# Kernel tuning notes

Hardware: AMD Instinct MI355X
Metric: run time of the kernel (lower is better)

The kernel has to match this reference:

```python
import jax, jax.numpy as jnp
import numpy as np

B, D = 16384, 1024
N_CROSS = 3
EPS = 1e-3  # keras BatchNormalization default epsilon


def _bn(x, gamma, beta, mean, var):
    # inference-mode batch norm over feature axis
    return gamma * (x - mean) * jax.lax.rsqrt(var + EPS) + beta


def setup_inputs() -> dict:
    key = jax.random.key(0)
    ks = jax.random.split(key, 16)
    s = lambda fan_in: 1.0 / np.sqrt(fan_in)
    inp = {
        "x": jax.random.normal(ks[0], (B, D), jnp.float32),
        "cross_w": jax.random.normal(ks[1], (N_CROSS, D), jnp.float32) * s(D),
        "cross_b": jax.random.normal(ks[2], (N_CROSS, D), jnp.float32) * 0.01,
        "w1": jax.random.normal(ks[3], (D, 64), jnp.float32) * s(D),
        "b1": jnp.zeros((64,), jnp.float32),
        "gamma1": jnp.ones((64,), jnp.float32),
        "beta1": jnp.zeros((64,), jnp.float32),
        "mean1": jax.random.normal(ks[4], (64,), jnp.float32) * 0.1,
        "var1": jax.random.uniform(ks[5], (64,), jnp.float32, 0.5, 1.5),
        "w2": jax.random.normal(ks[6], (64, 48), jnp.float32) * s(64),
        "b2": jnp.zeros((48,), jnp.float32),
        "gamma2": jnp.ones((48,), jnp.float32),
        "beta2": jnp.zeros((48,), jnp.float32),
        "mean2": jax.random.normal(ks[7], (48,), jnp.float32) * 0.1,
        "var2": jax.random.uniform(ks[8], (48,), jnp.float32, 0.5, 1.5),
        "w3": jax.random.normal(ks[9], (48, 24), jnp.float32) * s(48),
        "b3": jnp.zeros((24,), jnp.float32),
        "gamma3": jnp.ones((24,), jnp.float32),
        "beta3": jnp.zeros((24,), jnp.float32),
        "mean3": jax.random.normal(ks[10], (24,), jnp.float32) * 0.1,
        "var3": jax.random.uniform(ks[11], (24,), jnp.float32, 0.5, 1.5),
        "w_out": jax.random.normal(ks[12], (D + 24, 1), jnp.float32) * s(D + 24),
        "b_out": jnp.zeros((1,), jnp.float32),
    }
    return inp


def reference(x, cross_w, cross_b, w1, b1, gamma1, beta1, mean1, var1,
              w2, b2, gamma2, beta2, mean2, var2,
              w3, b3, gamma3, beta3, mean3, var3, w_out, b_out):
    # ---- cross network: xl = x0 * (xl . w) + b + xl ----
    # Algebraically identical to matmul(x0[:,:,None], xl[:,None,:]) @ w,
    # computed in O(B*D) instead of materializing [B, D, D].
    x0 = x
    xl = x
    for i in range(N_CROSS):
        scal = jnp.einsum('bd,d->b', xl, cross_w[i])  # [B]
        xl = x0 * scal[:, None] + cross_b[i] + xl
    # ---- deep tower (inference: dropout is identity, BN uses moving stats) ----
    h = _bn(jax.nn.relu(x @ w1 + b1), gamma1, beta1, mean1, var1)
    h = _bn(jnp.tanh(h @ w2 + b2), gamma2, beta2, mean2, var2)
    h = _bn(jnp.tanh(h @ w3 + b3), gamma3, beta3, mean3, var3)
    out = jnp.concatenate([xl, h], axis=1)           # [B, D+24]
    return jax.nn.sigmoid(out @ w_out + b_out)       # [B, 1]
```

## Files before the change

kernel.cpp:

```cpp
#include <hip/hip_runtime.h>
#include <hip/hip_bf16.h>
#include <math.h>

typedef __attribute__((ext_vector_type(8))) short bf16x8;
typedef __attribute__((ext_vector_type(4))) float f32x4;

constexpr int BD = 1024;
constexpr float EPS = 1e-3f;
constexpr int WB_MAIN = 32 * 5 * 64 * 8 * 2;
constexpr int WB2_OFF = WB_MAIN;
constexpr int WB3_OFF = WB2_OFF + 6144;
constexpr int CST_OFF = WB3_OFF + 4096;

__device__ __forceinline__ float wave_allsum(float v) {
#pragma unroll
    for (int m = 1; m < 64; m <<= 1) v += __shfl_xor(v, m, 64);
    return v;
}
__device__ __forceinline__ unsigned short f2bf(float f) {
    __hip_bfloat16 h = __float2bfloat16(f);
    unsigned short u; __builtin_memcpy(&u, &h, 2);
    return u;
}
__device__ __forceinline__ float bf2f(unsigned short u) {
    return __uint_as_float(((unsigned)u) << 16);
}
__device__ __forceinline__ float tanh_fast(float x) {
    const float xc = fminf(fmaxf(x, -15.f), 15.f);
    const float e = __expf(2.f * xc);
    return (e - 1.f) * __builtin_amdgcn_rcpf(e + 1.f);
}
__device__ __forceinline__ float sigmoid_fast(float z) {
    return __builtin_amdgcn_rcpf(1.f + __expf(-z));
}

__global__ void dcn_prep(const float* __restrict__ w1,
                         const float* __restrict__ cross_w,
                         const float* __restrict__ cross_b,
                         const float* __restrict__ w_out,
                         const float* __restrict__ w2,
                         const float* __restrict__ w3,
                         unsigned short* __restrict__ ws) {
    const int bx = blockIdx.x;
    if (bx == 40) {
        if (threadIdx.x < 64) {
            const int l = threadIdx.x;
            float q2 = 0.f, q3 = 0.f, Cc = 0.f;
            for (int j = 0; j < 16; ++j) {
                const int k = l * 16 + j;
                const float c0 = cross_b[k], c1 = cross_b[BD + k], c2 = cross_b[2 * BD + k];
                q2 += c0 * cross_w[BD + k];
                q3 += (c0 + c1) * cross_w[2 * BD + k];
                Cc += (c0 + c1 + c2) * w_out[k];
            }
            q2 = wave_allsum(q2); q3 = wave_allsum(q3); Cc = wave_allsum(Cc);
            float* consts = (float*)((char*)ws + CST_OFF);
            if (l == 0) { consts[0] = q2; consts[1] = q3; consts[2] = Cc; }
        }
        return;
    }
    if (bx < 40) {
        const int idx = bx * 256 + threadIdx.x;
        const int g = idx / 320;
        const int rem = idx - g * 320;
        const int t = rem >> 6;
        const int l = rem & 63;
        const int c = l & 15;
        const int k0 = g * 32 + (l >> 4) * 8;
        unsigned short o[8] __attribute__((aligned(16)));
#pragma unroll
        for (int j = 0; j < 8; ++j) {
            const int k = k0 + j;
            unsigned short r;
            if (t < 4) {
                r = f2bf(w1[k * 64 + t * 16 + c]);
            } else if (c < 8) {
                const int vsel = c & 3;
                const float v = (vsel < 3) ? cross_w[vsel * BD + k] : w_out[k];
                const unsigned short h = f2bf(v);
                r = (c < 4) ? h : f2bf(v - bf2f(h));
            } else {
                r = 0;
            }
            o[j] = r;
        }
        *(uint4*)(ws + (size_t)idx * 8) = *(const uint4*)o;
        return;
    }
    const int slot = (bx - 41) * 256 + threadIdx.x;
    if (slot < 384) {
        const int f = slot >> 6, l = slot & 63;
        const int K = f / 3, T = f % 3;
        const int kb = K * 32 + (l >> 4) * 8;
        const int col = T * 16 + (l & 15);
        unsigned short o[8] __attribute__((aligned(16)));
#pragma unroll
        for (int j = 0; j < 8; ++j) o[j] = f2bf(w2[(kb + j) * 48 + col]);
        unsigned short* wb2 = (unsigned short*)((char*)ws + WB2_OFF);
        *(uint4*)(wb2 + (size_t)slot * 8) = *(const uint4*)o;
    } else if (slot < 640) {
        const int s2 = slot - 384;
        const int f = s2 >> 6, l = s2 & 63;
        const int K = f >> 1, T = f & 1;
        const int kb = K * 32 + (l >> 4) * 8;
        const int col = T * 16 + (l & 15);
        unsigned short o[8] __attribute__((aligned(16)));
#pragma unroll
        for (int j = 0; j < 8; ++j) {
            const int k = kb + j;
            o[j] = (k < 48 && col < 24) ? f2bf(w3[k * 24 + col]) : (unsigned short)0;
        }
        unsigned short* wb3 = (unsigned short*)((char*)ws + WB3_OFF);
        *(uint4*)(wb3 + (size_t)s2 * 8) = *(const uint4*)o;
    }
}

__global__ __launch_bounds__(64, 1) void dcn_main(
    const float* __restrict__ x,
    const unsigned short* __restrict__ wbm,
    const unsigned short* __restrict__ w2f,
    const unsigned short* __restrict__ w3f,
    const float* __restrict__ consts,
    const float* __restrict__ b1, const float* __restrict__ g1,
    const float* __restrict__ be1, const float* __restrict__ m1, const float* __restrict__ v1,
    const float* __restrict__ b2, const float* __restrict__ g2,
    const float* __restrict__ be2, const float* __restrict__ m2, const float* __restrict__ v2,
    const float* __restrict__ b3, const float* __restrict__ g3,
    const float* __restrict__ be3, const float* __restrict__ m3, const float* __restrict__ v3,
    const float* __restrict__ w_out, const float* __restrict__ b_out,
    float* __restrict__ out)
{
    __shared__ char sb[8960] __attribute__((aligned(16)));
    constexpr int H1 = 0, H2 = 4352, LC = 8704;

    const int l = threadIdx.x;
    const int ar = l & 15;
    const int ag = l >> 4;
    const int gr0 = blockIdx.x * 16;

    const float* xbase = x + (size_t)(gr0 + ar) * BD + ag * 8;
    const bf16x8* bb = (const bf16x8*)wbm + l;

    const float q2c = consts[0], q3c = consts[1], Ccc = consts[2];
    const float bo = b_out[0];
    const float wo0 = w_out[1024 + ar];
    const float wo1 = (ar < 8) ? w_out[1040 + ar] : 0.f;
    float b1p[4], g1p[4], be1p[4], m1p[4], iv1p[4];
#pragma unroll
    for (int t = 0; t < 4; ++t) {
        const int c = t * 16 + ar;
        b1p[t] = b1[c]; g1p[t] = g1[c]; be1p[t] = be1[c]; m1p[t] = m1[c];
        iv1p[t] = rsqrtf(v1[c] + EPS);
    }

    float4 A0[6], A1[6];
#pragma unroll
    for (int s = 0; s < 6; ++s) {
        A0[s] = *(const float4*)(xbase + s * 32);
        A1[s] = *(const float4*)(xbase + s * 32 + 4);
    }
    bf16x8 Bf[4][5];
#pragma unroll
    for (int s = 0; s < 4; ++s)
#pragma unroll
        for (int t = 0; t < 5; ++t) Bf[s][t] = bb[(s * 5 + t) * 64];

    f32x4 acc0 = {0.f,0.f,0.f,0.f}, acc1 = acc0, acc2 = acc0, acc3 = acc0, acc4 = acc0;

#pragma unroll
    for (int s = 0; s < 32; ++s) {
        const float4 va0 = A0[s % 6];
        const float4 va1 = A1[s % 6];
        if (s + 6 < 32) {
            A0[s % 6] = *(const float4*)(xbase + (s + 6) * 32);
            A1[s % 6] = *(const float4*)(xbase + (s + 6) * 32 + 4);
        }
        const bf16x8 B0 = Bf[s & 3][0], B1 = Bf[s & 3][1], B2 = Bf[s & 3][2],
                     B3 = Bf[s & 3][3], B4 = Bf[s & 3][4];
        if (s + 4 < 32) {
#pragma unroll
            for (int t = 0; t < 5; ++t) Bf[s & 3][t] = bb[((s + 4) * 5 + t) * 64];
        }
        bf16x8 xh, xl;
#define CVT(F, I) { const unsigned short h_ = f2bf(F); xh[I] = (short)h_; \
                    xl[I] = (short)f2bf((F) - bf2f(h_)); }
        CVT(va0.x, 0) CVT(va0.y, 1) CVT(va0.z, 2) CVT(va0.w, 3)
        CVT(va1.x, 4) CVT(va1.y, 5) CVT(va1.z, 6) CVT(va1.w, 7)
#undef CVT
        acc0 = __builtin_amdgcn_mfma_f32_16x16x32_bf16(xh, B0, acc0, 0, 0, 0);
        acc1 = __builtin_amdgcn_mfma_f32_16x16x32_bf16(xh, B1, acc1, 0, 0, 0);
        acc2 = __builtin_amdgcn_mfma_f32_16x16x32_bf16(xh, B2, acc2, 0, 0, 0);
        acc3 = __builtin_amdgcn_mfma_f32_16x16x32_bf16(xh, B3, acc3, 0, 0, 0);
        acc4 = __builtin_amdgcn_mfma_f32_16x16x32_bf16(xh, B4, acc4, 0, 0, 0);
        acc4 = __builtin_amdgcn_mfma_f32_16x16x32_bf16(xl, B4, acc4, 0, 0, 0);
    }

    const bf16x8* w2b = (const bf16x8*)w2f + l;
    bf16x8 W2[6];
#pragma unroll
    for (int f = 0; f < 6; ++f) W2[f] = w2b[f * 64];
    const bf16x8* w3b = (const bf16x8*)w3f + l;
    bf16x8 W3[4];
#pragma unroll
    for (int f = 0; f < 4; ++f) W3[f] = w3b[f * 64];
    float b2p[3], g2p[3], be2p[3], m2p[3], iv2p[3];
#pragma unroll
    for (int t = 0; t < 3; ++t) {
        const int c = t * 16 + ar;
        b2p[t] = b2[c]; g2p[t] = g2[c]; be2p[t] = be2[c]; m2p[t] = m2[c];
        iv2p[t] = rsqrtf(v2[c] + EPS);
    }
    float b3p[2], g3p[2], be3p[2], m3p[2], iv3p[2];
#pragma unroll
    for (int t = 0; t < 2; ++t) {
        const int c = t == 0 ? ar : (16 + ar < 24 ? 16 + ar : 23);
        b3p[t] = b3[c]; g3p[t] = g3[c]; be3p[t] = be3[c]; m3p[t] = m3[c];
        iv3p[t] = rsqrtf(v3[c] + EPS);
    }

    {
        f32x4 p4 = acc4;
#pragma unroll
        for (int q = 0; q < 4; ++q) p4[q] += __shfl_xor(acc4[q], 4, 64);
        if (ar < 4) {
#pragma unroll
            for (int q = 0; q < 4; ++q)
                *(float*)&sb[LC + ((ag * 4 + q) * 4 + ar) * 4] = p4[q];
        }
    }

    {
        const f32x4 av[4] = {acc0, acc1, acc2, acc3};
#pragma unroll
        for (int t = 0; t < 4; ++t) {
            const int c = t * 16 + ar;
#pragma unroll
            for (int q = 0; q < 4; ++q) {
                const float y = fmaxf(av[t][q] + b1p[t], 0.f);
                const float h = fmaf(g1p[t] * (y - m1p[t]), iv1p[t], be1p[t]);
                *(float*)&sb[H1 + (ag * 4 + q) * 272 + c * 4] = h;
            }
        }
    }
    {
        const f32x4 z4 = {0.f, 0.f, 0.f, 0.f};
        *(f32x4*)&sb[H2 + ar * 272 + 192 + ag * 16] = z4;
    }

    bf16x8 a2[2];
#pragma unroll
    for (int K = 0; K < 2; ++K) {
        const float4 f0 = *(const float4*)&sb[H1 + ar * 272 + (K * 32 + ag * 8) * 4];
        const float4 f1 = *(const float4*)&sb[H1 + ar * 272 + (K * 32 + ag * 8) * 4 + 16];
        const float v[8] = {f0.x, f0.y, f0.z, f0.w, f1.x, f1.y, f1.z, f1.w};
#pragma unroll
        for (int i = 0; i < 8; ++i) a2[K][i] = (short)f2bf(v[i]);
    }
    f32x4 c2t[3] = {{0.f,0.f,0.f,0.f},{0.f,0.f,0.f,0.f},{0.f,0.f,0.f,0.f}};
#pragma unroll
    for (int K = 0; K < 2; ++K) {
        c2t[0] = __builtin_amdgcn_mfma_f32_16x16x32_bf16(a2[K], W2[K * 3 + 0], c2t[0], 0, 0, 0);
        c2t[1] = __builtin_amdgcn_mfma_f32_16x16x32_bf16(a2[K], W2[K * 3 + 1], c2t[1], 0, 0, 0);
        c2t[2] = __builtin_amdgcn_mfma_f32_16x16x32_bf16(a2[K], W2[K * 3 + 2], c2t[2], 0, 0, 0);
    }
#pragma unroll
    for (int t = 0; t < 3; ++t) {
        const int c = t * 16 + ar;
#pragma unroll
        for (int q = 0; q < 4; ++q) {
            const float th = tanh_fast(c2t[t][q] + b2p[t]);
            const float h = fmaf(g2p[t] * (th - m2p[t]), iv2p[t], be2p[t]);
            *(float*)&sb[H2 + (ag * 4 + q) * 272 + c * 4] = h;
        }
    }

    bf16x8 a3[2];
#pragma unroll
    for (int K = 0; K < 2; ++K) {
        const float4 f0 = *(const float4*)&sb[H2 + ar * 272 + (K * 32 + ag * 8) * 4];
        const float4 f1 = *(const float4*)&sb[H2 + ar * 272 + (K * 32 + ag * 8) * 4 + 16];
        const float v[8] = {f0.x, f0.y, f0.z, f0.w, f1.x, f1.y, f1.z, f1.w};
#pragma unroll
        for (int i = 0; i < 8; ++i) a3[K][i] = (short)f2bf(v[i]);
    }
    f32x4 c3t[2] = {{0.f,0.f,0.f,0.f},{0.f,0.f,0.f,0.f}};
#pragma unroll
    for (int K = 0; K < 2; ++K) {
        c3t[0] = __builtin_amdgcn_mfma_f32_16x16x32_bf16(a3[K], W3[K * 2 + 0], c3t[0], 0, 0, 0);
        c3t[1] = __builtin_amdgcn_mfma_f32_16x16x32_bf16(a3[K], W3[K * 2 + 1], c3t[1], 0, 0, 0);
    }
    float contrib[4];
#pragma unroll
    for (int q = 0; q < 4; ++q) {
        const float t0 = tanh_fast(c3t[0][q] + b3p[0]);
        const float h0 = fmaf(g3p[0] * (t0 - m3p[0]), iv3p[0], be3p[0]);
        const float t1 = tanh_fast(c3t[1][q] + b3p[1]);
        const float h1v = fmaf(g3p[1] * (t1 - m3p[1]), iv3p[1], be3p[1]);
        contrib[q] = h0 * wo0 + h1v * wo1;
    }
#pragma unroll
    for (int m = 1; m < 16; m <<= 1) {
#pragma unroll
        for (int q = 0; q < 4; ++q) contrib[q] += __shfl_xor(contrib[q], m, 64);
    }

#pragma unroll
    for (int q = 0; q < 4; ++q) {
        const f32x4 pr = *(const f32x4*)&sb[LC + (ag * 4 + q) * 16];
        const float p1 = pr[0], p2 = pr[1], p3 = pr[2], d0 = pr[3];
        const float s1 = p1;
        const float s2 = fmaf(1.f + s1, p2, q2c);
        const float s3 = fmaf(1.f + s1 + s2, p3, q3c);
        const float alpha = 1.f + s1 + s2 + s3;
        const float z = fmaf(alpha, d0, Ccc) + contrib[q] + bo;
        const float o = sigmoid_fast(z);
        if (ar == q) out[gr0 + ag * 4 + q] = o;
    }
}

extern "C" void kernel_launch(void* const* d_in, const int* in_sizes, int n_in,
                              void* d_out, int out_size, void* d_ws, size_t ws_size,
                              hipStream_t stream) {
    const float* x       = (const float*)d_in[0];
    const float* cross_w = (const float*)d_in[1];
    const float* cross_b = (const float*)d_in[2];
    const float* w1      = (const float*)d_in[3];
    const float* b1      = (const float*)d_in[4];
    const float* g1      = (const float*)d_in[5];
    const float* be1     = (const float*)d_in[6];
    const float* m1      = (const float*)d_in[7];
    const float* v1      = (const float*)d_in[8];
    const float* w2      = (const float*)d_in[9];
    const float* b2      = (const float*)d_in[10];
    const float* g2      = (const float*)d_in[11];
    const float* be2     = (const float*)d_in[12];
    const float* m2      = (const float*)d_in[13];
    const float* v2      = (const float*)d_in[14];
    const float* w3      = (const float*)d_in[15];
    const float* b3      = (const float*)d_in[16];
    const float* g3      = (const float*)d_in[17];
    const float* be3     = (const float*)d_in[18];
    const float* m3      = (const float*)d_in[19];
    const float* v3      = (const float*)d_in[20];
    const float* w_out   = (const float*)d_in[21];
    const float* b_out   = (const float*)d_in[22];
    float* out = (float*)d_out;

    unsigned short* ws = (unsigned short*)d_ws;
    const unsigned short* w2f = (const unsigned short*)((char*)d_ws + WB2_OFF);
    const unsigned short* w3f = (const unsigned short*)((char*)d_ws + WB3_OFF);
    const float* consts = (const float*)((char*)d_ws + CST_OFF);

    dcn_prep<<<44, 256, 0, stream>>>(w1, cross_w, cross_b, w_out, w2, w3, ws);
    dcn_main<<<1024, 64, 0, stream>>>(x, ws, w2f, w3f, consts,
                                      b1, g1, be1, m1, v1,
                                      b2, g2, be2, m2, v2,
                                      b3, g3, be3, m3, v3,
                                      w_out, b_out, out);
}
```

Measured before the change: 25.98 us.

## Split K dimension across two waves per block with LDS reduction

Each block now runs two wavefronts. Each wave processes half of the 1024-wide K dimension for the same 16 rows, and the second wave's MFMA accumulators are reduced into the first wave through shared memory before the tail stages run. This doubles the number of waves streaming x from memory and halves the serial MFMA chain per wave, aiming to hide load latency better. In exchange it adds an LDS round trip, a barrier, and a second wave that sits idle during the tail work.

```diff
diff --git a/kernel.cpp b/kernel.cpp
--- a/kernel.cpp
+++ b/kernel.cpp
@@ -115,7 +115,7 @@
     }
 }
 
-__global__ __launch_bounds__(64, 1) void dcn_main(
+__global__ __launch_bounds__(128, 2) void dcn_main(
     const float* __restrict__ x,
     const unsigned short* __restrict__ wbm,
     const unsigned short* __restrict__ w2f,
@@ -130,32 +130,22 @@
     const float* __restrict__ w_out, const float* __restrict__ b_out,
     float* __restrict__ out)
 {
-    __shared__ char sb[8960] __attribute__((aligned(16)));
-    constexpr int H1 = 0, H2 = 4352, LC = 8704;
-
-    const int l = threadIdx.x;
+    __shared__ char sb[14336] __attribute__((aligned(16)));
+    constexpr int RED = 0, H1 = 5120, H2 = 9472, LC = 13824;
+
+    const int tid = threadIdx.x;
+    const int l = tid & 63;
+    const int w = tid >> 6;
     const int ar = l & 15;
     const int ag = l >> 4;
     const int gr0 = blockIdx.x * 16;
 
-    const float* xbase = x + (size_t)(gr0 + ar) * BD + ag * 8;
-    const bf16x8* bb = (const bf16x8*)wbm + l;
-
-    const float q2c = consts[0], q3c = consts[1], Ccc = consts[2];
-    const float bo = b_out[0];
-    const float wo0 = w_out[1024 + ar];
-    const float wo1 = (ar < 8) ? w_out[1040 + ar] : 0.f;
-    float b1p[4], g1p[4], be1p[4], m1p[4], iv1p[4];
-#pragma unroll
-    for (int t = 0; t < 4; ++t) {
-        const int c = t * 16 + ar;
-        b1p[t] = b1[c]; g1p[t] = g1[c]; be1p[t] = be1[c]; m1p[t] = m1[c];
-        iv1p[t] = rsqrtf(v1[c] + EPS);
-    }
-
-    float4 A0[6], A1[6];
-#pragma unroll
-    for (int s = 0; s < 6; ++s) {
+    const float* xbase = x + (size_t)(gr0 + ar) * BD + w * 512 + ag * 8;
+    const bf16x8* bb = (const bf16x8*)wbm + (size_t)(w * 16 * 5) * 64 + l;
+
+    float4 A0[8], A1[8];
+#pragma unroll
+    for (int s = 0; s < 8; ++s) {
         A0[s] = *(const float4*)(xbase + s * 32);
         A1[s] = *(const float4*)(xbase + s * 32 + 4);
     }
@@ -168,16 +158,16 @@
     f32x4 acc0 = {0.f,0.f,0.f,0.f}, acc1 = acc0, acc2 = acc0, acc3 = acc0, acc4 = acc0;
 
 #pragma unroll
-    for (int s = 0; s < 32; ++s) {
-        const float4 va0 = A0[s % 6];
-        const float4 va1 = A1[s % 6];
-        if (s + 6 < 32) {
-            A0[s % 6] = *(const float4*)(xbase + (s + 6) * 32);
-            A1[s % 6] = *(const float4*)(xbase + (s + 6) * 32 + 4);
+    for (int s = 0; s < 16; ++s) {
+        const float4 va0 = A0[s & 7];
+        const float4 va1 = A1[s & 7];
+        if (s < 8) {
+            A0[s & 7] = *(const float4*)(xbase + (s + 8) * 32);
+            A1[s & 7] = *(const float4*)(xbase + (s + 8) * 32 + 4);
         }
         const bf16x8 B0 = Bf[s & 3][0], B1 = Bf[s & 3][1], B2 = Bf[s & 3][2],
                      B3 = Bf[s & 3][3], B4 = Bf[s & 3][4];
-        if (s + 4 < 32) {
+        if (s + 4 < 16) {
 #pragma unroll
             for (int t = 0; t < 5; ++t) Bf[s & 3][t] = bb[((s + 4) * 5 + t) * 64];
         }
@@ -195,6 +185,22 @@
         acc4 = __builtin_amdgcn_mfma_f32_16x16x32_bf16(xl, B4, acc4, 0, 0, 0);
     }
 
+    if (w == 1) {
+        *(f32x4*)&sb[RED + 0 * 1024 + l * 16] = acc0;
+        *(f32x4*)&sb[RED + 1 * 1024 + l * 16] = acc1;
+        *(f32x4*)&sb[RED + 2 * 1024 + l * 16] = acc2;
+        *(f32x4*)&sb[RED + 3 * 1024 + l * 16] = acc3;
+        *(f32x4*)&sb[RED + 4 * 1024 + l * 16] = acc4;
+    }
+    __syncthreads();
+    if (w == 1) return;
+
+    acc0 += *(const f32x4*)&sb[RED + 0 * 1024 + l * 16];
+    acc1 += *(const f32x4*)&sb[RED + 1 * 1024 + l * 16];
+    acc2 += *(const f32x4*)&sb[RED + 2 * 1024 + l * 16];
+    acc3 += *(const f32x4*)&sb[RED + 3 * 1024 + l * 16];
+    acc4 += *(const f32x4*)&sb[RED + 4 * 1024 + l * 16];
+
     const bf16x8* w2b = (const bf16x8*)w2f + l;
     bf16x8 W2[6];
 #pragma unroll
@@ -203,6 +209,18 @@
     bf16x8 W3[4];
 #pragma unroll
     for (int f = 0; f < 4; ++f) W3[f] = w3b[f * 64];
+
+    const float q2c = consts[0], q3c = consts[1], Ccc = consts[2];
+    const float bo = b_out[0];
+    const float wo0 = w_out[1024 + ar];
+    const float wo1 = (ar < 8) ? w_out[1040 + ar] : 0.f;
+    float b1p[4], g1p[4], be1p[4], m1p[4], iv1p[4];
+#pragma unroll
+    for (int t = 0; t < 4; ++t) {
+        const int c = t * 16 + ar;
+        b1p[t] = b1[c]; g1p[t] = g1[c]; be1p[t] = be1[c]; m1p[t] = m1[c];
+        iv1p[t] = rsqrtf(v1[c] + EPS);
+    }
     float b2p[3], g2p[3], be2p[3], m2p[3], iv2p[3];
 #pragma unroll
     for (int t = 0; t < 3; ++t) {
@@ -352,9 +370,9 @@
     const float* consts = (const float*)((char*)d_ws + CST_OFF);
 
     dcn_prep<<<44, 256, 0, stream>>>(w1, cross_w, cross_b, w_out, w2, w3, ws);
-    dcn_main<<<1024, 64, 0, stream>>>(x, ws, w2f, w3f, consts,
-                                      b1, g1, be1, m1, v1,
-                                      b2, g2, be2, m2, v2,
-                                      b3, g3, be3, m3, v3,
-                                      w_out, b_out, out);
-}
+    dcn_main<<<1024, 128, 0, stream>>>(x, ws, w2f, w3f, consts,
+                                       b1, g1, be1, m1, v1,
+                                       b2, g2, be2, m2, v2,
+                                       b3, g3, be3, m3, v3,
+                                       w_out, b_out, out);
+}
```

Result: no change. 26.18 us (+0.8%).
